# Kernel tuning notes

Hardware: AMD Instinct MI355X
Metric: run time of the kernel (lower is better)

## Reference

```python
import jax, jax.numpy as jnp
import numpy as np

E = 1024  # embedding_size
H = 16    # multi_head_num


def setup_inputs() -> dict:
    key = jax.random.key(0)
    ks = jax.random.split(key, 9)
    B, N = 4, 1024
    s = 1.0 / np.sqrt(E)
    return {
        "x": jax.random.normal(ks[0], (B, N, E), dtype=jnp.float32),
        "Wq": jax.random.normal(ks[1], (E, E), dtype=jnp.float32) * s,
        "bq": jax.random.normal(ks[2], (E,), dtype=jnp.float32) * 0.02,
        "Wk": jax.random.normal(ks[3], (E, E), dtype=jnp.float32) * s,
        "bk": jax.random.normal(ks[4], (E,), dtype=jnp.float32) * 0.02,
        "Wv": jax.random.normal(ks[5], (E, E), dtype=jnp.float32) * s,
        "bv": jax.random.normal(ks[6], (E,), dtype=jnp.float32) * 0.02,
        "Wo": jax.random.normal(ks[7], (E, E), dtype=jnp.float32) * s,
        "bo": jax.random.normal(ks[8], (E,), dtype=jnp.float32) * 0.02,
    }


def reference(x, Wq, bq, Wk, bk, Wv, bv, Wo, bo):
    B, N, _ = x.shape
    d = E // H

    def heads(y):  # [B,N,E] -> [B,H,N,d]
        return y.reshape(B, N, H, d).transpose(0, 2, 1, 3)

    q = heads(x @ Wq.T + bq)
    k = heads(x @ Wk.T + bk)
    v = heads(x @ Wv.T + bv)

    energy = jnp.einsum('bhqd,bhkd->bhqk', q, k)
    # NOTE: module divides by sqrt(E) AFTER softmax (faithful to source)
    scaling = jnp.asarray(E, x.dtype) ** 0.5
    att = jax.nn.softmax(energy, axis=-1) / scaling
    out = jnp.einsum('bhal,bhlv->bhav', att, v)
    out = out.transpose(0, 2, 1, 3).reshape(B, N, E)
    return out @ Wo.T + bo
```

## Files before the change

kernel.cpp:

```cpp
#include <hip/hip_runtime.h>
#include <hip/hip_bf16.h>


typedef __bf16 bf16x8 __attribute__((ext_vector_type(8)));
typedef __bf16 bf16x4 __attribute__((ext_vector_type(4)));
typedef float  f32x4  __attribute__((ext_vector_type(4)));

#define LOG2E 1.44269504f

__device__ __forceinline__ void glds16(const __bf16* g, __bf16* l) {
  __builtin_amdgcn_global_load_lds(
      (const __attribute__((address_space(1))) void*)g,
      (__attribute__((address_space(3))) void*)l, 16, 0, 0);
}

__global__ __launch_bounds__(256) void cvt_f32_bf16(const float* __restrict__ in,
                                                    __bf16* __restrict__ out, int n4) {
  int i = blockIdx.x * 256 + threadIdx.x;
  if (i < n4) {
    float4 v = *(const float4*)(in + (size_t)i * 4);
    bf16x4 b = {(__bf16)v.x, (__bf16)v.y, (__bf16)v.z, (__bf16)v.w};
    *(bf16x4*)(out + (size_t)i * 4) = b;
  }
}

__global__ __launch_bounds__(256) void cvt_all(const float* __restrict__ x,
                                               const float* __restrict__ Wq,
                                               const float* __restrict__ Wk,
                                               const float* __restrict__ Wv,
                                               const float* __restrict__ Wo,
                                               __bf16* __restrict__ xb,
                                               __bf16* __restrict__ Wqb,
                                               __bf16* __restrict__ Wkb,
                                               __bf16* __restrict__ Wvb,
                                               __bf16* __restrict__ Wob) {
  const int i = blockIdx.x * 256 + threadIdx.x;
  const float* src;
  __bf16* dst;
  int off;
  if (i < 1048576) {
    src = x; dst = xb; off = i;
  } else {
    const int j = i - 1048576;
    const int seg = j >> 18;
    off = j & 262143;
    src = (seg == 0) ? Wq : (seg == 1) ? Wk : (seg == 2) ? Wv : Wo;
    dst = (seg == 0) ? Wqb : (seg == 1) ? Wkb : (seg == 2) ? Wvb : Wob;
  }
  float4 v = *(const float4*)(src + (size_t)off * 4);
  bf16x4 b = {(__bf16)v.x, (__bf16)v.y, (__bf16)v.z, (__bf16)v.w};
  *(bf16x4*)(dst + (size_t)off * 4) = b;
}

template <bool WBF16>
__global__ __launch_bounds__(256, 3) void gemm_qkv(const __bf16* __restrict__ A,
                                                   const void* __restrict__ Wqp,
                                                   const void* __restrict__ Wkp,
                                                   const void* __restrict__ Wvp,
                                                   const float* __restrict__ bq,
                                                   const float* __restrict__ bk,
                                                   const float* __restrict__ bv,
                                                   __bf16* __restrict__ Qw,
                                                   __bf16* __restrict__ Kw,
                                                   __bf16* __restrict__ Vw) {
  constexpr int BST = WBF16 ? 64 : 72;
  __shared__ __attribute__((aligned(16))) __bf16 As[128][64];
  __shared__ __attribute__((aligned(16))) __bf16 Bs[128 * BST];

  const int tid = threadIdx.x;
  const int lane = tid & 63, w = tid >> 6;
  const int wm = w >> 1, wn = w & 1;
  const int l15 = lane & 15, lq = lane >> 4;
  const int lr = lane >> 3, lc = lane & 7;
  const int xs = l15 & 7;

  const int bid = blockIdx.x;
  const int c = bid & 7, t = bid >> 3;
  const int z = t >> 5;
  const int r = t & 31;
  const int nb = r & 7;
  const int mb = c * 4 + (r >> 3);
  const int m0 = mb * 128, n0 = nb * 128;

  const void* Wp = (z == 0) ? Wqp : (z == 1) ? Wkp : Wvp;
  const float* bias = (z == 0) ? bq : (z == 1) ? bk : bv;
  __bf16* C = (z == 0) ? Qw : (z == 1) ? Kw : Vw;
  const float scale = (z == 0) ? LOG2E : 1.0f;

  f32x4 acc[4][4] = {};

  for (int k0 = 0; k0 < 1024; k0 += 64) {
#pragma unroll
    for (int i = 0; i < 4; ++i) {
      const int row = w * 32 + i * 8 + lr;
      glds16(A + (size_t)(m0 + row) * 1024 + k0 + ((lc ^ lr) * 8), &As[row][lc * 8]);
    }
    if (WBF16) {
      const __bf16* Wb = (const __bf16*)Wp;
#pragma unroll
      for (int i = 0; i < 4; ++i) {
        const int row = w * 32 + i * 8 + lr;
        glds16(Wb + (size_t)(n0 + row) * 1024 + k0 + ((lc ^ lr) * 8), &Bs[row * 64 + lc * 8]);
      }
    } else {
      const float* W = (const float*)Wp;
#pragma unroll
      for (int i = 0; i < 8; ++i) {
        const int cc = i * 256 + tid, row = cc >> 4, col = (cc & 15) * 4;
        float4 wv = *(const float4*)(W + (size_t)(n0 + row) * 1024 + k0 + col);
        bf16x4 b4 = {(__bf16)wv.x, (__bf16)wv.y, (__bf16)wv.z, (__bf16)wv.w};
        *(bf16x4*)(&Bs[row * 72 + col]) = b4;
      }
    }
    __syncthreads();
#pragma unroll
    for (int s = 0; s < 2; ++s) {
      bf16x8 af[4], bfv[4];
#pragma unroll
      for (int mt = 0; mt < 4; ++mt)
        af[mt] = *(const bf16x8*)(&As[wm * 64 + mt * 16 + l15][((s * 4 + lq) ^ xs) * 8]);
#pragma unroll
      for (int nt = 0; nt < 4; ++nt) {
        const int row = wn * 64 + nt * 16 + l15;
        if (WBF16)
          bfv[nt] = *(const bf16x8*)(&Bs[row * 64 + (((s * 4 + lq) ^ xs) * 8)]);
        else
          bfv[nt] = *(const bf16x8*)(&Bs[row * 72 + s * 32 + lq * 8]);
      }
#pragma unroll
      for (int mt = 0; mt < 4; ++mt)
#pragma unroll
        for (int nt = 0; nt < 4; ++nt)
          acc[mt][nt] = __builtin_amdgcn_mfma_f32_16x16x32_bf16(
              af[mt], bfv[nt], acc[mt][nt], 0, 0, 0);
    }
    __syncthreads();
  }

#pragma unroll
  for (int mt = 0; mt < 4; ++mt) {
    const int mg_base = m0 + wm * 64 + mt * 16 + lq * 4;
    const int bb = mg_base >> 10, nr0 = mg_base & 1023;
#pragma unroll
    for (int nt = 0; nt < 4; ++nt) {
      const int ng = n0 + wn * 64 + nt * 16 + l15;
      const float bv = bias[ng];
      const int h = ng >> 6, dd = ng & 63;
      if (z != 2) {
#pragma unroll
        for (int rr = 0; rr < 4; ++rr) {
          const int mg = mg_base + rr;
          const size_t idx =
              ((size_t)(bb * 16 + h) << 16) + (size_t)(mg & 1023) * 64 + dd;
          C[idx] = (__bf16)((acc[mt][nt][rr] + bv) * scale);
        }
      } else {
        bf16x4 o4 = {(__bf16)(acc[mt][nt][0] + bv), (__bf16)(acc[mt][nt][1] + bv),
                     (__bf16)(acc[mt][nt][2] + bv), (__bf16)(acc[mt][nt][3] + bv)};
        *(bf16x4*)(&C[((size_t)(bb * 16 + h) << 16) + (size_t)dd * 1024 + nr0]) = o4;
      }
    }
  }
}

__global__ __launch_bounds__(256) void gemm_out(const __bf16* __restrict__ A,
                                                const __bf16* __restrict__ W,
                                                const float* __restrict__ bias,
                                                float* __restrict__ C) {
  __shared__ __attribute__((aligned(16))) __bf16 As[32][64];
  __shared__ __attribute__((aligned(16))) __bf16 Bs[128][64];

  const int tid = threadIdx.x;
  const int lane = tid & 63, w = tid >> 6;
  const int wm = w >> 1, wn = w & 1;
  const int l15 = lane & 15, lq = lane >> 4;
  const int lr = lane >> 3, lc = lane & 7;
  const int xs = l15 & 7;
  const int m0 = blockIdx.x * 32, n0 = blockIdx.y * 128;

  f32x4 acc[4] = {};

  for (int k0 = 0; k0 < 1024; k0 += 64) {
    {
      const int row = w * 8 + lr;
      glds16(A + (size_t)(m0 + row) * 1024 + k0 + ((lc ^ lr) * 8), &As[row][lc * 8]);
    }
#pragma unroll
    for (int i = 0; i < 4; ++i) {
      const int row = w * 32 + i * 8 + lr;
      glds16(W + (size_t)(n0 + row) * 1024 + k0 + ((lc ^ lr) * 8), &Bs[row][lc * 8]);
    }
    __syncthreads();
#pragma unroll
    for (int s = 0; s < 2; ++s) {
      bf16x8 af = *(const bf16x8*)(&As[wm * 16 + l15][((s * 4 + lq) ^ xs) * 8]);
#pragma unroll
      for (int nt = 0; nt < 4; ++nt) {
        bf16x8 bfv = *(const bf16x8*)(&Bs[wn * 64 + nt * 16 + l15][((s * 4 + lq) ^ xs) * 8]);
        acc[nt] = __builtin_amdgcn_mfma_f32_16x16x32_bf16(af, bfv, acc[nt], 0, 0, 0);
      }
    }
    __syncthreads();
  }

  const int mg_base = m0 + wm * 16 + lq * 4;
#pragma unroll
  for (int nt = 0; nt < 4; ++nt) {
    const int ng = n0 + wn * 64 + nt * 16 + l15;
    const float bv = bias[ng];
#pragma unroll
    for (int r = 0; r < 4; ++r)
      C[(size_t)(mg_base + r) * 1024 + ng] = acc[nt][r] + bv;
  }
}

__global__ __launch_bounds__(256) void attn_kernel(const __bf16* __restrict__ Q,
                                                   const __bf16* __restrict__ K,
                                                   const __bf16* __restrict__ Vt,
                                                   __bf16* __restrict__ O) {
  __shared__ __attribute__((aligned(16))) __bf16 Qs[64][64];
  __shared__ __attribute__((aligned(16))) __bf16 Ks[64][64];
  __shared__ __attribute__((aligned(16))) __bf16 Vs[64][64];
  __shared__ __attribute__((aligned(16))) __bf16 Ps[4][16][72];

  const int tid = threadIdx.x;
  const int lane = tid & 63, w = tid >> 6;
  const int l15 = lane & 15, lq = lane >> 4;
  const int lr = lane >> 3, lc = lane & 7;
  const int xs = l15 & 7;

  const int bh = blockIdx.x;
  const int qt = blockIdx.y;
  const __bf16* Qh = Q + (size_t)bh * 65536;
  const __bf16* Kh = K + (size_t)bh * 65536;
  const __bf16* Vh = Vt + (size_t)bh * 65536;

#pragma unroll
  for (int i = 0; i < 2; ++i) {
    const int row = w * 16 + i * 8 + lr;
    glds16(Qh + (size_t)(qt * 64 + row) * 64 + ((lc ^ lr) * 8), &Qs[row][lc * 8]);
  }
  __syncthreads();
  bf16x8 bqr[2];
#pragma unroll
  for (int s = 0; s < 2; ++s)
    bqr[s] = *(const bf16x8*)(&Qs[w * 16 + l15][((s * 4 + lq) ^ xs) * 8]);

  float l_run = 0.0f;
  f32x4 oacc[4] = {};

  for (int kb = 0; kb < 16; ++kb) {
#pragma unroll
    for (int i = 0; i < 2; ++i) {
      const int row = w * 16 + i * 8 + lr;
      glds16(Kh + (size_t)kb * 4096 + (size_t)row * 64 + ((lc ^ lr) * 8), &Ks[row][lc * 8]);
      glds16(Vh + (size_t)row * 1024 + kb * 64 + ((lc ^ lr) * 8), &Vs[row][lc * 8]);
    }
    __syncthreads();

    f32x4 sacc[4] = {};
#pragma unroll
    for (int s = 0; s < 2; ++s) {
#pragma unroll
      for (int mt = 0; mt < 4; ++mt) {
        bf16x8 ak = *(const bf16x8*)(&Ks[mt * 16 + l15][((s * 4 + lq) ^ xs) * 8]);
        sacc[mt] = __builtin_amdgcn_mfma_f32_16x16x32_bf16(ak, bqr[s], sacc[mt], 0, 0, 0);
      }
    }

    float sum = 0.0f;
#pragma unroll
    for (int mt = 0; mt < 4; ++mt)
#pragma unroll
      for (int r = 0; r < 4; ++r) {
        const float e = __builtin_amdgcn_exp2f(sacc[mt][r]);
        sacc[mt][r] = e;
        sum += e;
      }
    sum += __shfl_xor(sum, 16, 64);
    sum += __shfl_xor(sum, 32, 64);
    l_run += sum;

#pragma unroll
    for (int mt = 0; mt < 4; ++mt) {
      bf16x4 p4 = {(__bf16)sacc[mt][0], (__bf16)sacc[mt][1],
                   (__bf16)sacc[mt][2], (__bf16)sacc[mt][3]};
      *(bf16x4*)(&Ps[w][l15][mt * 16 + lq * 4]) = p4;
    }
    __threadfence_block();

#pragma unroll
    for (int s = 0; s < 2; ++s) {
      bf16x8 bp = *(const bf16x8*)(&Ps[w][l15][s * 32 + lq * 8]);
#pragma unroll
      for (int mt = 0; mt < 4; ++mt) {
        bf16x8 av = *(const bf16x8*)(&Vs[mt * 16 + l15][((s * 4 + lq) ^ xs) * 8]);
        oacc[mt] = __builtin_amdgcn_mfma_f32_16x16x32_bf16(av, bp, oacc[mt], 0, 0, 0);
      }
    }
    __syncthreads();
  }

  const int b = bh >> 4, h = bh & 15;
  const float inv = 1.0f / (l_run * 32.0f);
  const size_t base = (size_t)(b * 1024 + qt * 64 + w * 16 + l15) * 1024 + h * 64;
#pragma unroll
  for (int mt = 0; mt < 4; ++mt) {
    bf16x4 o4 = {(__bf16)(oacc[mt][0] * inv), (__bf16)(oacc[mt][1] * inv),
                 (__bf16)(oacc[mt][2] * inv), (__bf16)(oacc[mt][3] * inv)};
    *(bf16x4*)(&O[base + mt * 16 + lq * 4]) = o4;
  }
}

extern "C" void kernel_launch(void* const* d_in, const int* in_sizes, int n_in,
                              void* d_out, int out_size, void* d_ws, size_t ws_size,
                              hipStream_t stream) {
  const float* x  = (const float*)d_in[0];
  const float* Wq = (const float*)d_in[1];
  const float* bq = (const float*)d_in[2];
  const float* Wk = (const float*)d_in[3];
  const float* bk = (const float*)d_in[4];
  const float* Wv = (const float*)d_in[5];
  const float* bv = (const float*)d_in[6];
  const float* Wo = (const float*)d_in[7];
  const float* bo = (const float*)d_in[8];
  float* out = (float*)d_out;

  const size_t SZ = (size_t)4 * 1024 * 1024;
  __bf16* Qw = (__bf16*)d_ws;
  __bf16* Kw = Qw + SZ;
  __bf16* Vw = Kw + SZ;
  __bf16* s3 = Vw + SZ;
  __bf16* xb = s3;
  __bf16* Ow = s3;

  dim3 blk(256);

  if (ws_size >= (size_t)40 * 1024 * 1024) {
    __bf16* Wqb = s3 + SZ;
    __bf16* Wkb = Wqb + SZ / 4;
    __bf16* Wvb = Wkb + SZ / 4;
    __bf16* Wob = Wvb + SZ / 4;
    cvt_all<<<8192, blk, 0, stream>>>(x, Wq, Wk, Wv, Wo, xb, Wqb, Wkb, Wvb, Wob);
    gemm_qkv<true><<<dim3(768), blk, 0, stream>>>(xb, Wqb, Wkb, Wvb,
                                                  bq, bk, bv, Qw, Kw, Vw);
    attn_kernel<<<dim3(64, 16), blk, 0, stream>>>(Qw, Kw, Vw, Ow);
    gemm_out<<<dim3(128, 8), blk, 0, stream>>>(Ow, Wob, bo, out);
  } else {
    __bf16* Wob = Kw;
    cvt_f32_bf16<<<4096, blk, 0, stream>>>(x, xb, 1048576);
    gemm_qkv<false><<<dim3(768), blk, 0, stream>>>(xb, Wq, Wk, Wv,
                                                   bq, bk, bv, Qw, Kw, Vw);
    attn_kernel<<<dim3(64, 16), blk, 0, stream>>>(Qw, Kw, Vw, Ow);
    cvt_f32_bf16<<<1024, blk, 0, stream>>>(Wo, Wob, 262144);
    gemm_out<<<dim3(128, 8), blk, 0, stream>>>(Ow, Wob, bo, out);
  }
}
```

Measured before the change: 171.8 us.

## Double per-block tile sizes in attention and output GEMM with swizzled block order

The attention kernel now processes 128 queries per block (32 per wave), so each K/V tile staged in LDS is reused across twice as many query rows. The Q staging buffer is aliased with the P scratch buffer to keep LDS use down. The output GEMM moves from 32x128 to 64x128 tiles with a 1D grid remapped so neighbouring blocks share A/W panels for L2 locality. The aim is less global and LDS traffic per FLOP, paid for with fewer blocks (512 each), which reduces occupancy and wave-level parallelism on a large-CU GPU.

```diff
diff --git a/kernel.cpp b/kernel.cpp
--- a/kernel.cpp
+++ b/kernel.cpp
@@ -167,7 +167,7 @@
                                                 const __bf16* __restrict__ W,
                                                 const float* __restrict__ bias,
                                                 float* __restrict__ C) {
-  __shared__ __attribute__((aligned(16))) __bf16 As[32][64];
+  __shared__ __attribute__((aligned(16))) __bf16 As[64][64];
   __shared__ __attribute__((aligned(16))) __bf16 Bs[128][64];
 
   const int tid = threadIdx.x;
@@ -176,13 +176,19 @@
   const int l15 = lane & 15, lq = lane >> 4;
   const int lr = lane >> 3, lc = lane & 7;
   const int xs = l15 & 7;
-  const int m0 = blockIdx.x * 32, n0 = blockIdx.y * 128;
-
-  f32x4 acc[4] = {};
+
+  const int bid = blockIdx.x;
+  const int c = bid & 7, t = bid >> 3;
+  const int mb = c * 8 + (t & 7);
+  const int nb = t >> 3;
+  const int m0 = mb * 64, n0 = nb * 128;
+
+  f32x4 acc[2][4] = {};
 
   for (int k0 = 0; k0 < 1024; k0 += 64) {
-    {
-      const int row = w * 8 + lr;
+#pragma unroll
+    for (int i = 0; i < 2; ++i) {
+      const int row = w * 16 + i * 8 + lr;
       glds16(A + (size_t)(m0 + row) * 1024 + k0 + ((lc ^ lr) * 8), &As[row][lc * 8]);
     }
 #pragma unroll
@@ -193,24 +199,34 @@
     __syncthreads();
 #pragma unroll
     for (int s = 0; s < 2; ++s) {
-      bf16x8 af = *(const bf16x8*)(&As[wm * 16 + l15][((s * 4 + lq) ^ xs) * 8]);
-#pragma unroll
-      for (int nt = 0; nt < 4; ++nt) {
-        bf16x8 bfv = *(const bf16x8*)(&Bs[wn * 64 + nt * 16 + l15][((s * 4 + lq) ^ xs) * 8]);
-        acc[nt] = __builtin_amdgcn_mfma_f32_16x16x32_bf16(af, bfv, acc[nt], 0, 0, 0);
-      }
-    }
-    __syncthreads();
-  }
-
-  const int mg_base = m0 + wm * 16 + lq * 4;
-#pragma unroll
-  for (int nt = 0; nt < 4; ++nt) {
-    const int ng = n0 + wn * 64 + nt * 16 + l15;
-    const float bv = bias[ng];
-#pragma unroll
-    for (int r = 0; r < 4; ++r)
-      C[(size_t)(mg_base + r) * 1024 + ng] = acc[nt][r] + bv;
+      bf16x8 af[2], bfv[4];
+#pragma unroll
+      for (int mt = 0; mt < 2; ++mt)
+        af[mt] = *(const bf16x8*)(&As[wm * 32 + mt * 16 + l15][((s * 4 + lq) ^ xs) * 8]);
+#pragma unroll
+      for (int nt = 0; nt < 4; ++nt)
+        bfv[nt] = *(const bf16x8*)(&Bs[wn * 64 + nt * 16 + l15][((s * 4 + lq) ^ xs) * 8]);
+#pragma unroll
+      for (int mt = 0; mt < 2; ++mt)
+#pragma unroll
+        for (int nt = 0; nt < 4; ++nt)
+          acc[mt][nt] = __builtin_amdgcn_mfma_f32_16x16x32_bf16(
+              af[mt], bfv[nt], acc[mt][nt], 0, 0, 0);
+    }
+    __syncthreads();
+  }
+
+#pragma unroll
+  for (int mt = 0; mt < 2; ++mt) {
+    const int mg_base = m0 + wm * 32 + mt * 16 + lq * 4;
+#pragma unroll
+    for (int nt = 0; nt < 4; ++nt) {
+      const int ng = n0 + wn * 64 + nt * 16 + l15;
+      const float bv = bias[ng];
+#pragma unroll
+      for (int r = 0; r < 4; ++r)
+        C[(size_t)(mg_base + r) * 1024 + ng] = acc[mt][nt][r] + bv;
+    }
   }
 }
 
@@ -218,10 +234,12 @@
                                                    const __bf16* __restrict__ K,
                                                    const __bf16* __restrict__ Vt,
                                                    __bf16* __restrict__ O) {
-  __shared__ __attribute__((aligned(16))) __bf16 Qs[64][64];
+  __shared__ __attribute__((aligned(16))) __bf16 PQ[9216];
   __shared__ __attribute__((aligned(16))) __bf16 Ks[64][64];
   __shared__ __attribute__((aligned(16))) __bf16 Vs[64][64];
-  __shared__ __attribute__((aligned(16))) __bf16 Ps[4][16][72];
+
+  __bf16(*Qst)[64] = (__bf16(*)[64])PQ;
+  __bf16(*Ps)[32][72] = (__bf16(*)[32][72])PQ;
 
   const int tid = threadIdx.x;
   const int lane = tid & 63, w = tid >> 6;
@@ -236,18 +254,20 @@
   const __bf16* Vh = Vt + (size_t)bh * 65536;
 
 #pragma unroll
-  for (int i = 0; i < 2; ++i) {
-    const int row = w * 16 + i * 8 + lr;
-    glds16(Qh + (size_t)(qt * 64 + row) * 64 + ((lc ^ lr) * 8), &Qs[row][lc * 8]);
+  for (int i = 0; i < 4; ++i) {
+    const int row = w * 32 + i * 8 + lr;
+    glds16(Qh + (size_t)(qt * 128 + row) * 64 + ((lc ^ lr) * 8), &Qst[row][lc * 8]);
   }
   __syncthreads();
-  bf16x8 bqr[2];
-#pragma unroll
-  for (int s = 0; s < 2; ++s)
-    bqr[s] = *(const bf16x8*)(&Qs[w * 16 + l15][((s * 4 + lq) ^ xs) * 8]);
-
-  float l_run = 0.0f;
-  f32x4 oacc[4] = {};
+  bf16x8 bqr[2][2];
+#pragma unroll
+  for (int nq = 0; nq < 2; ++nq)
+#pragma unroll
+    for (int s = 0; s < 2; ++s)
+      bqr[nq][s] = *(const bf16x8*)(&Qst[w * 32 + nq * 16 + l15][((s * 4 + lq) ^ xs) * 8]);
+
+  float l_run[2] = {0.0f, 0.0f};
+  f32x4 oacc[2][4] = {};
 
   for (int kb = 0; kb < 16; ++kb) {
 #pragma unroll
@@ -258,57 +278,75 @@
     }
     __syncthreads();
 
-    f32x4 sacc[4] = {};
+    f32x4 sacc[2][4] = {};
 #pragma unroll
     for (int s = 0; s < 2; ++s) {
 #pragma unroll
       for (int mt = 0; mt < 4; ++mt) {
         bf16x8 ak = *(const bf16x8*)(&Ks[mt * 16 + l15][((s * 4 + lq) ^ xs) * 8]);
-        sacc[mt] = __builtin_amdgcn_mfma_f32_16x16x32_bf16(ak, bqr[s], sacc[mt], 0, 0, 0);
-      }
-    }
-
-    float sum = 0.0f;
-#pragma unroll
-    for (int mt = 0; mt < 4; ++mt)
-#pragma unroll
-      for (int r = 0; r < 4; ++r) {
-        const float e = __builtin_amdgcn_exp2f(sacc[mt][r]);
-        sacc[mt][r] = e;
-        sum += e;
-      }
-    sum += __shfl_xor(sum, 16, 64);
-    sum += __shfl_xor(sum, 32, 64);
-    l_run += sum;
-
-#pragma unroll
-    for (int mt = 0; mt < 4; ++mt) {
-      bf16x4 p4 = {(__bf16)sacc[mt][0], (__bf16)sacc[mt][1],
-                   (__bf16)sacc[mt][2], (__bf16)sacc[mt][3]};
-      *(bf16x4*)(&Ps[w][l15][mt * 16 + lq * 4]) = p4;
-    }
+#pragma unroll
+        for (int nq = 0; nq < 2; ++nq)
+          sacc[nq][mt] = __builtin_amdgcn_mfma_f32_16x16x32_bf16(
+              ak, bqr[nq][s], sacc[nq][mt], 0, 0, 0);
+      }
+    }
+
+#pragma unroll
+    for (int nq = 0; nq < 2; ++nq) {
+      float sum = 0.0f;
+#pragma unroll
+      for (int mt = 0; mt < 4; ++mt)
+#pragma unroll
+        for (int r = 0; r < 4; ++r) {
+          const float e = __builtin_amdgcn_exp2f(sacc[nq][mt][r]);
+          sacc[nq][mt][r] = e;
+          sum += e;
+        }
+      sum += __shfl_xor(sum, 16, 64);
+      sum += __shfl_xor(sum, 32, 64);
+      l_run[nq] += sum;
+    }
+
+#pragma unroll
+    for (int nq = 0; nq < 2; ++nq)
+#pragma unroll
+      for (int mt = 0; mt < 4; ++mt) {
+        bf16x4 p4 = {(__bf16)sacc[nq][mt][0], (__bf16)sacc[nq][mt][1],
+                     (__bf16)sacc[nq][mt][2], (__bf16)sacc[nq][mt][3]};
+        *(bf16x4*)(&Ps[w][nq * 16 + l15][mt * 16 + lq * 4]) = p4;
+      }
     __threadfence_block();
 
 #pragma unroll
     for (int s = 0; s < 2; ++s) {
-      bf16x8 bp = *(const bf16x8*)(&Ps[w][l15][s * 32 + lq * 8]);
+      bf16x8 bp[2];
+#pragma unroll
+      for (int nq = 0; nq < 2; ++nq)
+        bp[nq] = *(const bf16x8*)(&Ps[w][nq * 16 + l15][s * 32 + lq * 8]);
 #pragma unroll
       for (int mt = 0; mt < 4; ++mt) {
         bf16x8 av = *(const bf16x8*)(&Vs[mt * 16 + l15][((s * 4 + lq) ^ xs) * 8]);
-        oacc[mt] = __builtin_amdgcn_mfma_f32_16x16x32_bf16(av, bp, oacc[mt], 0, 0, 0);
+#pragma unroll
+        for (int nq = 0; nq < 2; ++nq)
+          oacc[nq][mt] = __builtin_amdgcn_mfma_f32_16x16x32_bf16(
+              av, bp[nq], oacc[nq][mt], 0, 0, 0);
       }
     }
     __syncthreads();
   }
 
   const int b = bh >> 4, h = bh & 15;
-  const float inv = 1.0f / (l_run * 32.0f);
-  const size_t base = (size_t)(b * 1024 + qt * 64 + w * 16 + l15) * 1024 + h * 64;
-#pragma unroll
-  for (int mt = 0; mt < 4; ++mt) {
-    bf16x4 o4 = {(__bf16)(oacc[mt][0] * inv), (__bf16)(oacc[mt][1] * inv),
-                 (__bf16)(oacc[mt][2] * inv), (__bf16)(oacc[mt][3] * inv)};
-    *(bf16x4*)(&O[base + mt * 16 + lq * 4]) = o4;
+#pragma unroll
+  for (int nq = 0; nq < 2; ++nq) {
+    const float inv = 1.0f / (l_run[nq] * 32.0f);
+    const size_t base =
+        (size_t)(b * 1024 + qt * 128 + w * 32 + nq * 16 + l15) * 1024 + h * 64;
+#pragma unroll
+    for (int mt = 0; mt < 4; ++mt) {
+      bf16x4 o4 = {(__bf16)(oacc[nq][mt][0] * inv), (__bf16)(oacc[nq][mt][1] * inv),
+                   (__bf16)(oacc[nq][mt][2] * inv), (__bf16)(oacc[nq][mt][3] * inv)};
+      *(bf16x4*)(&O[base + mt * 16 + lq * 4]) = o4;
+    }
   }
 }
 
@@ -344,15 +382,15 @@
     cvt_all<<<8192, blk, 0, stream>>>(x, Wq, Wk, Wv, Wo, xb, Wqb, Wkb, Wvb, Wob);
     gemm_qkv<true><<<dim3(768), blk, 0, stream>>>(xb, Wqb, Wkb, Wvb,
                                                   bq, bk, bv, Qw, Kw, Vw);
-    attn_kernel<<<dim3(64, 16), blk, 0, stream>>>(Qw, Kw, Vw, Ow);
-    gemm_out<<<dim3(128, 8), blk, 0, stream>>>(Ow, Wob, bo, out);
+    attn_kernel<<<dim3(64, 8), blk, 0, stream>>>(Qw, Kw, Vw, Ow);
+    gemm_out<<<dim3(512), blk, 0, stream>>>(Ow, Wob, bo, out);
   } else {
     __bf16* Wob = Kw;
     cvt_f32_bf16<<<4096, blk, 0, stream>>>(x, xb, 1048576);
     gemm_qkv<false><<<dim3(768), blk, 0, stream>>>(xb, Wq, Wk, Wv,
                                                    bq, bk, bv, Qw, Kw, Vw);
-    attn_kernel<<<dim3(64, 16), blk, 0, stream>>>(Qw, Kw, Vw, Ow);
+    attn_kernel<<<dim3(64, 8), blk, 0, stream>>>(Qw, Kw, Vw, Ow);
     cvt_f32_bf16<<<1024, blk, 0, stream>>>(Wo, Wob, 262144);
-    gemm_out<<<dim3(128, 8), blk, 0, stream>>>(Ow, Wob, bo, out);
-  }
-}
+    gemm_out<<<dim3(512), blk, 0, stream>>>(Ow, Wob, bo, out);
+  }
+}
```

Result: faster. 164.6 us (-4.2%).
